# Performance work log

Measured on AMD Instinct MI355X. Metric: run time of the kernel, lower is better.

## Reference

```python
import jax, jax.numpy as jnp
import numpy as np

B = 262144
PI = float(np.pi)

# Panda DH constants (theta is the joint variable): columns (d, a, alpha)
_D  = np.array([0.333, 0.0, 0.316, 0.0, 0.384, 0.0, 0.107], dtype=np.float32)
_A  = np.array([0.0, 0.0, 0.0, 0.0825, -0.0825, 0.0, 0.088], dtype=np.float32)
_AL = np.array([0.0, -PI/2, PI/2, PI/2, -PI/2, PI/2, PI/2], dtype=np.float32)


def setup_inputs() -> dict:
    key = jax.random.key(0)
    k1, k2 = jax.random.split(key)
    joints = jax.random.normal(k1, (B, 7), dtype=jnp.float32)
    poses = jax.random.normal(k2, (B, 6), dtype=jnp.float32)
    return {"joints": joints, "poses": poses}


def _fk_pose(joints):
    # joints: [B,7] -> [B,6] (xyz position + XYZ Euler angles)
    d = jnp.asarray(_D)
    a = jnp.asarray(_A)
    al = jnp.asarray(_AL)
    ct, st = jnp.cos(joints), jnp.sin(joints)          # [B,7]
    cal, sal = jnp.cos(al), jnp.sin(al)                # [7]
    zeros = jnp.zeros_like(ct)
    ones = jnp.ones_like(ct)
    # A matrices, batched over B and joint index: [B,7,4,4]
    r0 = jnp.stack([ct, -st * cal, st * sal, a * ct], axis=-1)
    r1 = jnp.stack([st, ct * cal, -ct * sal, a * st], axis=-1)
    r2 = jnp.stack([zeros, sal * ones, cal * ones, d * ones], axis=-1)
    r3 = jnp.stack([zeros, zeros, zeros, ones], axis=-1)
    A = jnp.stack([r0, r1, r2, r3], axis=-2)           # [B,7,4,4]
    # Chain of 4x4 transforms: T = A0 @ A1 @ ... @ A6
    T = A[:, 0]
    for i in range(1, 7):
        T = jnp.einsum('bij,bjk->bik', T, A[:, i])
    pos = T[:, :3, 3]                                   # [B,3]
    R = T[:, :3, :3]
    # matrix_to_euler_angles(R, 'XYZ'):
    #   [atan2(-R12, R22), asin(R02), atan2(-R01, R00)]
    rpy = jnp.stack([
        jnp.arctan2(-R[:, 1, 2], R[:, 2, 2]),
        jnp.arcsin(R[:, 0, 2]),
        jnp.arctan2(-R[:, 0, 1], R[:, 0, 0]),
    ], axis=-1)                                         # [B,3]
    return jnp.concatenate([pos, rpy], axis=-1)         # [B,6]


def reference(joints, poses):
    joints_fk = _fk_pose(joints)
    return jnp.mean((joints_fk - poses) ** 2)
```

## Files before the change

kernel.cpp:

```cpp
#include <hip/hip_runtime.h>


#define FK_B 262144
#define NBLK (FK_B / 256)

__device__ __forceinline__ float fast_atan2f(float y, float x) {
    const float ax = fabsf(x), ay = fabsf(y);
    const float mx = fmaxf(ax, ay);
    const float mn = fminf(ax, ay);
    float t = __fdividef(mn, fmaxf(mx, 1e-30f));
    const bool red = t > 0.41421356f;
    const float tr = __fdividef(t - 1.0f, t + 1.0f);
    float u = red ? tr : t;
    const float s = u * u;
    float p = fmaf(s, 8.05374449538e-2f, -1.38776856032e-1f);
    p = fmaf(s, p, 1.99777106478e-1f);
    p = fmaf(s, p, -3.33329491539e-1f);
    float r = fmaf(u * s, p, u);
    if (red) r += 0.78539816340f;
    if (ay > ax) r = 1.57079632679f - r;
    if (x < 0.0f) r = 3.14159265359f - r;
    return copysignf(r, y);
}

__device__ __forceinline__ void dh_step(float R[3][3], float p[3],
                                        float ct, float st,
                                        float d, float a,
                                        float cal, float sal) {
    const float c0x = ct,        c0y = st,        c0z = 0.0f;
    const float c1x = -st * cal, c1y = ct * cal,  c1z = sal;
    const float c2x = st * sal,  c2y = -ct * sal, c2z = cal;
    const float px = a * ct, py = a * st, pz = d;

    float nR[3][3], np[3];
#pragma unroll
    for (int r = 0; r < 3; ++r) {
        nR[r][0] = R[r][0] * c0x + R[r][1] * c0y + R[r][2] * c0z;
        nR[r][1] = R[r][0] * c1x + R[r][1] * c1y + R[r][2] * c1z;
        nR[r][2] = R[r][0] * c2x + R[r][1] * c2y + R[r][2] * c2z;
        np[r]    = R[r][0] * px  + R[r][1] * py  + R[r][2] * pz + p[r];
    }
#pragma unroll
    for (int r = 0; r < 3; ++r) {
        R[r][0] = nR[r][0]; R[r][1] = nR[r][1]; R[r][2] = nR[r][2];
        p[r] = np[r];
    }
}

__global__ __launch_bounds__(256) void fk_loss_kernel(
    const float* __restrict__ joints,
    const float* __restrict__ poses,
    float* __restrict__ partials)
{
    const int i = blockIdx.x * blockDim.x + threadIdx.x;

    float s[7], c[7];
#pragma unroll
    for (int k = 0; k < 7; ++k) {
        const float q = joints[i * 7 + k];
        s[k] = __sinf(q);
        c[k] = __cosf(q);
    }

    float R[3][3] = {{c[0], -s[0], 0.0f},
                     {s[0],  c[0], 0.0f},
                     {0.0f,  0.0f, 1.0f}};
    float p[3] = {0.0f, 0.0f, 0.333f};

    dh_step(R, p, c[1], s[1], 0.0f,   0.0f,    0.0f, -1.0f);
    dh_step(R, p, c[2], s[2], 0.316f, 0.0f,    0.0f,  1.0f);
    dh_step(R, p, c[3], s[3], 0.0f,   0.0825f, 0.0f,  1.0f);
    dh_step(R, p, c[4], s[4], 0.384f,-0.0825f, 0.0f, -1.0f);
    dh_step(R, p, c[5], s[5], 0.0f,   0.0f,    0.0f,  1.0f);
    dh_step(R, p, c[6], s[6], 0.107f, 0.088f,  0.0f,  1.0f);

    float fk[6];
    fk[0] = p[0]; fk[1] = p[1]; fk[2] = p[2];
    fk[3] = fast_atan2f(-R[1][2], R[2][2]);
    const float r02 = fminf(1.0f, fmaxf(-1.0f, R[0][2]));
    fk[4] = fast_atan2f(r02, sqrtf(fmaxf(0.0f, 1.0f - r02 * r02)));
    fk[5] = fast_atan2f(-R[0][1], R[0][0]);

    float err = 0.0f;
#pragma unroll
    for (int k = 0; k < 6; ++k) {
        float dlt = fk[k] - poses[i * 6 + k];
        err += dlt * dlt;
    }

#pragma unroll
    for (int off = 32; off > 0; off >>= 1)
        err += __shfl_down(err, off, 64);

    __shared__ float wsum[4];
    const int lane = threadIdx.x & 63;
    const int wid  = threadIdx.x >> 6;
    if (lane == 0) wsum[wid] = err;
    __syncthreads();
    if (threadIdx.x == 0)
        partials[blockIdx.x] = wsum[0] + wsum[1] + wsum[2] + wsum[3];
}

__global__ __launch_bounds__(256) void fk_reduce_kernel(
    const float* __restrict__ partials,
    float* __restrict__ out)
{
    const int t = threadIdx.x;
    float v = 0.0f;
#pragma unroll
    for (int k = 0; k < NBLK / 256; ++k)
        v += partials[t + k * 256];

#pragma unroll
    for (int off = 32; off > 0; off >>= 1)
        v += __shfl_down(v, off, 64);

    __shared__ float wsum[4];
    const int lane = t & 63;
    const int wid  = t >> 6;
    if (lane == 0) wsum[wid] = v;
    __syncthreads();
    if (t == 0)
        out[0] = (wsum[0] + wsum[1] + wsum[2] + wsum[3]) * (1.0f / (FK_B * 6.0f));
}

extern "C" void kernel_launch(void* const* d_in, const int* in_sizes, int n_in,
                              void* d_out, int out_size, void* d_ws, size_t ws_size,
                              hipStream_t stream) {
    const float* joints = (const float*)d_in[0];
    const float* poses  = (const float*)d_in[1];
    float* out      = (float*)d_out;
    float* partials = (float*)d_ws;

    fk_loss_kernel<<<NBLK, 256, 0, stream>>>(joints, poses, partials);
    fk_reduce_kernel<<<1, 256, 0, stream>>>(partials, out);
}
```

Baseline: 66.44 us.

## Fuse loss and reduction into cooperative kernel and stage inputs via LDS

After: 131.3 us. 1.98x slower.

```diff
diff --git a/kernel.cpp b/kernel.cpp
--- a/kernel.cpp
+++ b/kernel.cpp
@@ -1,4 +1,7 @@
 #include <hip/hip_runtime.h>
+#include <hip/hip_cooperative_groups.h>
+
+namespace cg = cooperative_groups;
 
 
 #define FK_B 262144
@@ -47,17 +50,29 @@
     }
 }
 
-__global__ __launch_bounds__(256) void fk_loss_kernel(
+__global__ __launch_bounds__(256) void fk_loss_fused(
     const float* __restrict__ joints,
     const float* __restrict__ poses,
-    float* __restrict__ partials)
+    float* __restrict__ partials,
+    float* __restrict__ out)
 {
-    const int i = blockIdx.x * blockDim.x + threadIdx.x;
+    const int t   = threadIdx.x;
+    const int bid = blockIdx.x;
+
+    __shared__ float4 j4[448];
+    __shared__ float4 p4[384];
+    const float4* jg = (const float4*)joints + bid * 448;
+    const float4* pg = (const float4*)poses  + bid * 384;
+    for (int k = t; k < 448; k += 256) j4[k] = jg[k];
+    for (int k = t; k < 384; k += 256) p4[k] = pg[k];
+    __syncthreads();
+    const float* j_lds = (const float*)j4;
+    const float* p_lds = (const float*)p4;
 
     float s[7], c[7];
 #pragma unroll
     for (int k = 0; k < 7; ++k) {
-        const float q = joints[i * 7 + k];
+        const float q = j_lds[t * 7 + k];
         s[k] = __sinf(q);
         c[k] = __cosf(q);
     }
@@ -84,7 +99,7 @@
     float err = 0.0f;
 #pragma unroll
     for (int k = 0; k < 6; ++k) {
-        float dlt = fk[k] - poses[i * 6 + k];
+        float dlt = fk[k] - p_lds[t * 6 + k];
         err += dlt * dlt;
     }
 
@@ -93,35 +108,30 @@
         err += __shfl_down(err, off, 64);
 
     __shared__ float wsum[4];
-    const int lane = threadIdx.x & 63;
-    const int wid  = threadIdx.x >> 6;
+    const int lane = t & 63;
+    const int wid  = t >> 6;
     if (lane == 0) wsum[wid] = err;
     __syncthreads();
-    if (threadIdx.x == 0)
-        partials[blockIdx.x] = wsum[0] + wsum[1] + wsum[2] + wsum[3];
-}
+    if (t == 0) {
+        partials[bid] = wsum[0] + wsum[1] + wsum[2] + wsum[3];
+        __threadfence();
+    }
 
-__global__ __launch_bounds__(256) void fk_reduce_kernel(
-    const float* __restrict__ partials,
-    float* __restrict__ out)
-{
-    const int t = threadIdx.x;
-    float v = 0.0f;
+    cg::this_grid().sync();
+
+    if (bid == 0) {
+        const float4* pp = (const float4*)partials;
+        const float4 v4 = pp[t];
+        float v = (v4.x + v4.y) + (v4.z + v4.w);
 #pragma unroll
-    for (int k = 0; k < NBLK / 256; ++k)
-        v += partials[t + k * 256];
-
-#pragma unroll
-    for (int off = 32; off > 0; off >>= 1)
-        v += __shfl_down(v, off, 64);
-
-    __shared__ float wsum[4];
-    const int lane = t & 63;
-    const int wid  = t >> 6;
-    if (lane == 0) wsum[wid] = v;
-    __syncthreads();
-    if (t == 0)
-        out[0] = (wsum[0] + wsum[1] + wsum[2] + wsum[3]) * (1.0f / (FK_B * 6.0f));
+        for (int off = 32; off > 0; off >>= 1)
+            v += __shfl_down(v, off, 64);
+        __shared__ float fsum[4];
+        if (lane == 0) fsum[wid] = v;
+        __syncthreads();
+        if (t == 0)
+            out[0] = (fsum[0] + fsum[1] + fsum[2] + fsum[3]) * (1.0f / (FK_B * 6.0f));
+    }
 }
 
 extern "C" void kernel_launch(void* const* d_in, const int* in_sizes, int n_in,
@@ -132,6 +142,7 @@
     float* out      = (float*)d_out;
     float* partials = (float*)d_ws;
 
-    fk_loss_kernel<<<NBLK, 256, 0, stream>>>(joints, poses, partials);
-    fk_reduce_kernel<<<1, 256, 0, stream>>>(partials, out);
+    void* args[] = {(void*)&joints, (void*)&poses, (void*)&partials, (void*)&out};
+    hipLaunchCooperativeKernel((const void*)fk_loss_fused,
+                               dim3(NBLK), dim3(256), args, 0, stream);
 }
```
